# Performance work log

Hardware: AMD Instinct MI355X
Metric: run time of the kernel (lower is better)

The kernel has to match this reference:

```python
import jax, jax.numpy as jnp
import numpy as np

N = 50000        # node_num
E = 1600000      # num edges (avg degree 32)
IN_DIM = 128
OUT_DIM = 64
SLOPE = 0.1      # leaky relu slope_ratio
EPS = 1e-12


def setup_inputs() -> dict:
    key = jax.random.key(0)
    k0, k1, k2, k3 = jax.random.split(key, 4)
    x = jax.random.normal(k0, (N, IN_DIM), dtype=jnp.float32)
    edge_index = jax.random.randint(k1, (2, E), 0, N, dtype=jnp.int64)
    # Linear(in_dim, out_dim) params
    W = jax.random.normal(k2, (OUT_DIM, IN_DIM), dtype=jnp.float32) * (1.0 / np.sqrt(IN_DIM))
    b = jnp.zeros((OUT_DIM,), dtype=jnp.float32)
    # attention vector a: [2*out_dim, 1], kaiming-normal-ish init
    a = jax.random.normal(k3, (2 * OUT_DIM, 1), dtype=jnp.float32) * np.sqrt(2.0 / (2 * OUT_DIM))
    return {"x": x, "edge_index": edge_index, "W": W, "b": b, "a": a}


def reference(x, edge_index, W, b, a):
    # new_embeddings = Linear(x)
    new = x @ W.T + b                          # [N, OUT_DIM]
    src = edge_index[0]
    dst = edge_index[1]
    # cat(new[src], new[dst]) @ a  ==  new[src]@a_src + new[dst]@a_dst (avoids [E, 2*OUT] intermediate)
    a_src = a[:OUT_DIM, 0]                     # [OUT_DIM]
    a_dst = a[OUT_DIM:, 0]                     # [OUT_DIM]
    score = new[src] @ a_src + new[dst] @ a_dst  # [E]
    e = jnp.exp(jax.nn.leaky_relu(score, SLOPE))  # [E]
    # spmm(A, ones) -> per-row sum of edge weights; spmm(A, new) -> weighted aggregation
    row_sum = jax.ops.segment_sum(e, src, num_segments=N)                 # [N]
    results = jax.ops.segment_sum(e[:, None] * new[dst], src, num_segments=N)  # [N, OUT_DIM]
    return results / (row_sum[:, None] + EPS)
```

## Files before the change

### kernel.cpp

```cpp
#include <hip/hip_runtime.h>
#include <hip/hip_bf16.h>

#define NN    50000
#define EE    1600000
#define IND   128
#define OUTD  64
#define SLOPE 0.1f

#define BSH    5
#define BW     32
#define NB     1564
#define NFINE  1568
#define CAP    1408
#define CAPT   6
#define CSH    8
#define NC     196
#define CAP1   8832
#define NBLK1  500
#define CHUNK1 (EE / NBLK1)
#define NSPLIT 4
#define SCAP   (CAP1 / NSPLIT)
#define NLIN   (NN / 16)

typedef __attribute__((ext_vector_type(8))) short short8;
typedef __attribute__((ext_vector_type(4))) float float4v;

union SMem {
    struct {
        ushort xs[16 * 136];
        ushort wt[64 * 136];
        float  newt[16 * 68];
    } lin;
    int h[NC];
};

__global__ __launch_bounds__(256) void fused_lincoarse_kernel(
    const float* __restrict__ x, const float* __restrict__ W,
    const float* __restrict__ bias, const float* __restrict__ a,
    const int* __restrict__ ei, int* __restrict__ gcur1,
    unsigned* __restrict__ ebuf1,
    ushort* __restrict__ nbuf2, float* __restrict__ s_src, float* __restrict__ s_dst)
{
    __shared__ SMem sm;
    const int tid = threadIdx.x;

    if (blockIdx.x < NBLK1) {
        int* h = sm.h;
        for (int i = tid; i < NC; i += 256) h[i] = 0;
        __syncthreads();
        const int base = blockIdx.x * CHUNK1;
        const int4* s4p = (const int4*)(ei + base);
        for (int i = tid; i < CHUNK1 / 4; i += 256) {
            int4 s4 = s4p[i];
            atomicAdd(&h[s4.x >> CSH], 1);
            atomicAdd(&h[s4.y >> CSH], 1);
            atomicAdd(&h[s4.z >> CSH], 1);
            atomicAdd(&h[s4.w >> CSH], 1);
        }
        __syncthreads();
        for (int i = tid; i < NC; i += 256) {
            int c = h[i];
            if (c) h[i] = i * CAP1 + atomicAdd(&gcur1[i * 16], c);
        }
        __syncthreads();
        const int4* d4p = (const int4*)(ei + EE + base);
        for (int i = tid; i < CHUNK1 / 4; i += 256) {
            int4 s4 = s4p[i];
            int4 d4 = d4p[i];
            int p0 = atomicAdd(&h[s4.x >> CSH], 1);
            int p1 = atomicAdd(&h[s4.y >> CSH], 1);
            int p2 = atomicAdd(&h[s4.z >> CSH], 1);
            int p3 = atomicAdd(&h[s4.w >> CSH], 1);
            ebuf1[p0] = ((unsigned)(s4.x & 255) << 16) | (unsigned)d4.x;
            ebuf1[p1] = ((unsigned)(s4.y & 255) << 16) | (unsigned)d4.y;
            ebuf1[p2] = ((unsigned)(s4.z & 255) << 16) | (unsigned)d4.z;
            ebuf1[p3] = ((unsigned)(s4.w & 255) << 16) | (unsigned)d4.w;
        }
        return;
    }

    const int node0 = (blockIdx.x - NBLK1) * 16;
    const float4* W4 = (const float4*)W;
    #pragma unroll
    for (int i = 0; i < 8; ++i) {
        int idx = tid + i * 256;
        float4 wv = W4[idx];
        int n = idx >> 5, k = (idx & 31) * 4;
        ushort4 pk; __hip_bfloat16 h;
        h = __float2bfloat16(wv.x); pk.x = *(ushort*)&h;
        h = __float2bfloat16(wv.y); pk.y = *(ushort*)&h;
        h = __float2bfloat16(wv.z); pk.z = *(ushort*)&h;
        h = __float2bfloat16(wv.w); pk.w = *(ushort*)&h;
        *(ushort4*)&sm.lin.wt[n * 136 + k] = pk;
    }
    const float4* x4 = (const float4*)(x + (size_t)node0 * IND);
    #pragma unroll
    for (int i = 0; i < 2; ++i) {
        int idx = tid + i * 256;
        float4 xv = x4[idx];
        int r = idx >> 5, cc = (idx & 31) * 4;
        ushort4 pk; __hip_bfloat16 h;
        h = __float2bfloat16(xv.x); pk.x = *(ushort*)&h;
        h = __float2bfloat16(xv.y); pk.y = *(ushort*)&h;
        h = __float2bfloat16(xv.z); pk.z = *(ushort*)&h;
        h = __float2bfloat16(xv.w); pk.w = *(ushort*)&h;
        *(ushort4*)&sm.lin.xs[r * 136 + cc] = pk;
    }
    __syncthreads();

    const int w    = tid >> 6;
    const int lane = tid & 63;
    const int q    = lane >> 4;
    const int m16  = lane & 15;
    float4v acc = {0.f, 0.f, 0.f, 0.f};
    #pragma unroll
    for (int kk = 0; kk < IND; kk += 32) {
        short8 af = *(const short8*)&sm.lin.xs[m16 * 136 + kk + q * 8];
        short8 bf = *(const short8*)&sm.lin.wt[(w * 16 + m16) * 136 + kk + q * 8];
        acc = __builtin_amdgcn_mfma_f32_16x16x32_bf16(af, bf, acc, 0, 0, 0);
    }
    const float bv = bias[w * 16 + m16];
    #pragma unroll
    for (int r = 0; r < 4; ++r)
        sm.lin.newt[(q * 4 + r) * 68 + w * 16 + m16] = acc[r] + bv;
    __syncthreads();

    const int nl = tid >> 4;
    const int jg = tid & 15;
    const int j0 = jg * 4;
    float4 va = *(const float4*)&sm.lin.newt[nl * 68 + j0];
    const int n = node0 + nl;
    ushort4 pk;
    { __hip_bfloat16 h;
      h = __float2bfloat16(va.x); pk.x = *(ushort*)&h;
      h = __float2bfloat16(va.y); pk.y = *(ushort*)&h;
      h = __float2bfloat16(va.z); pk.z = *(ushort*)&h;
      h = __float2bfloat16(va.w); pk.w = *(ushort*)&h; }
    *(ushort4*)&nbuf2[(size_t)n * OUTD + j0] = pk;

    float ss = va.x * a[j0]        + va.y * a[j0 + 1]
             + va.z * a[j0 + 2]    + va.w * a[j0 + 3];
    float sd = va.x * a[OUTD + j0]     + va.y * a[OUTD + j0 + 1]
             + va.z * a[OUTD + j0 + 2] + va.w * a[OUTD + j0 + 3];
    #pragma unroll
    for (int m = 1; m < 16; m <<= 1) {
        ss += __shfl_xor(ss, m, 64);
        sd += __shfl_xor(sd, m, 64);
    }
    if (jg == 0) { s_src[n] = ss; s_dst[n] = sd; }
}

__global__ __launch_bounds__(256) void finebin_kernel(
    const unsigned* __restrict__ ebuf1, const int* __restrict__ gcur1,
    int* __restrict__ gcur2, unsigned* __restrict__ ebuf2)
{
    __shared__ unsigned stage[SCAP];
    __shared__ int h[8], lofs[8], grun[8], cur[8];
    const int tid = threadIdx.x;
    const int c   = blockIdx.x >> 2;
    const int sp  = blockIdx.x & 3;
    const int cnt1 = gcur1[c * 16];
    const int seg  = (cnt1 + NSPLIT - 1) / NSPLIT;
    const int lo   = sp * seg;
    const int m    = max(0, min(cnt1, lo + seg) - lo);
    if (tid < 8) h[tid] = 0;
    __syncthreads();
    const unsigned* eb = ebuf1 + (size_t)c * CAP1 + lo;
    for (int i = tid; i < m; i += 256)
        atomicAdd(&h[eb[i] >> 21], 1);
    __syncthreads();
    if (tid == 0) {
        int run = 0;
        #pragma unroll
        for (int f = 0; f < 8; ++f) { lofs[f] = run; run += h[f]; }
    }
    __syncthreads();
    if (tid < 8) {
        cur[tid]  = lofs[tid];
        grun[tid] = atomicAdd(&gcur2[(c * 8 + tid) * 16], h[tid]);
    }
    __syncthreads();
    for (int i = tid; i < m; i += 256) {
        unsigned e = eb[i];
        int pos = atomicAdd(&cur[e >> 21], 1);
        stage[pos] = (((e >> 16) & 31u) << 16) | (e & 0xFFFFu);
    }
    __syncthreads();
    #pragma unroll 1
    for (int f = 0; f < 8; ++f) {
        const int cf = h[f];
        unsigned* dst = ebuf2 + (size_t)(c * 8 + f) * CAP + grun[f];
        const unsigned* sp2 = stage + lofs[f];
        for (int i = tid; i < cf; i += 256) dst[i] = sp2[i];
    }
}

__global__ __launch_bounds__(256) void aggregate_kernel(
    const unsigned* __restrict__ ebuf, const int* __restrict__ gcur,
    const ushort* __restrict__ nbuf2,
    const float* __restrict__ s_src, const float* __restrict__ s_dst,
    float* __restrict__ out)
{
    __shared__ uint2 pairs[CAP];
    __shared__ float ssL[BW];
    __shared__ int cntL[BW], ofs[BW], cur[BW];
    const int tid  = threadIdx.x;
    const int wid  = tid >> 6;
    const int lane = tid & 63;
    const int b    = blockIdx.x;
    const int n0   = b << BSH;
    const uint2* __restrict__ nbufq = (const uint2*)nbuf2;

    if (tid < BW) {
        int n = n0 + tid;
        ssL[tid]  = (n < NN) ? s_src[n] : 0.f;
        cntL[tid] = 0;
    }
    __syncthreads();

    const int cnt = gcur[b * 16];
    const unsigned* eb = ebuf + (size_t)b * CAP;

    unsigned er[CAPT]; float evr[CAPT];
    int nk = 0;
    for (int i = tid; i < cnt; i += 256) {
        unsigned e = eb[i];
        int d  = e & 0xFFFFu;
        int ln = e >> 16;
        float sc = ssL[ln] + s_dst[d];
        float lr = sc > 0.f ? sc : SLOPE * sc;
        er[nk] = e; evr[nk] = __expf(lr); ++nk;
        atomicAdd(&cntL[ln], 1);
    }
    __syncthreads();

    if (wid == 0) {
        int c = (lane < BW) ? cntL[lane] : 0;
        int sc = c;
        #pragma unroll
        for (int m = 1; m < BW; m <<= 1) {
            int v = __shfl_up(sc, m, 64);
            if (lane >= m) sc += v;
        }
        if (lane < BW) { ofs[lane] = sc - c; cur[lane] = sc - c; }
    }
    __syncthreads();

    for (int k = 0; k < nk; ++k) {
        int ln = er[k] >> 16;
        int pos = atomicAdd(&cur[ln], 1);
        pairs[pos] = make_uint2(er[k] & 0xFFFFu, __float_as_uint(evr[k]));
    }
    __syncthreads();

    const int e16 = lane >> 4;
    const int c16 = lane & 15;

    #pragma unroll 1
    for (int t = 0; t < BW / 4; ++t) {
        const int ln  = wid * (BW / 4) + t;
        const int beg = ofs[ln];
        const int len = cntL[ln];

        float a0 = 0.f, a1 = 0.f, a2 = 0.f, a3 = 0.f, es = 0.f;
        int j = 0;
        for (; j + 16 <= len; j += 16) {
            uint2 pA = pairs[beg + j + 0  + e16];
            uint2 pB = pairs[beg + j + 4  + e16];
            uint2 pC = pairs[beg + j + 8  + e16];
            uint2 pD = pairs[beg + j + 12 + e16];
            uint2 gA = nbufq[pA.x * 16 + c16];
            uint2 gB = nbufq[pB.x * 16 + c16];
            uint2 gC = nbufq[pC.x * 16 + c16];
            uint2 gD = nbufq[pD.x * 16 + c16];
            float fA = __uint_as_float(pA.y), fB = __uint_as_float(pB.y);
            float fC = __uint_as_float(pC.y), fD = __uint_as_float(pD.y);
            es += fA + fB + fC + fD;
            a0 = fmaf(fA, __uint_as_float(gA.x << 16), a0);
            a1 = fmaf(fA, __uint_as_float(gA.x & 0xFFFF0000u), a1);
            a2 = fmaf(fA, __uint_as_float(gA.y << 16), a2);
            a3 = fmaf(fA, __uint_as_float(gA.y & 0xFFFF0000u), a3);
            a0 = fmaf(fB, __uint_as_float(gB.x << 16), a0);
            a1 = fmaf(fB, __uint_as_float(gB.x & 0xFFFF0000u), a1);
            a2 = fmaf(fB, __uint_as_float(gB.y << 16), a2);
            a3 = fmaf(fB, __uint_as_float(gB.y & 0xFFFF0000u), a3);
            a0 = fmaf(fC, __uint_as_float(gC.x << 16), a0);
            a1 = fmaf(fC, __uint_as_float(gC.x & 0xFFFF0000u), a1);
            a2 = fmaf(fC, __uint_as_float(gC.y << 16), a2);
            a3 = fmaf(fC, __uint_as_float(gC.y & 0xFFFF0000u), a3);
            a0 = fmaf(fD, __uint_as_float(gD.x << 16), a0);
            a1 = fmaf(fD, __uint_as_float(gD.x & 0xFFFF0000u), a1);
            a2 = fmaf(fD, __uint_as_float(gD.y << 16), a2);
            a3 = fmaf(fD, __uint_as_float(gD.y & 0xFFFF0000u), a3);
        }
        for (; j < len; j += 4) {
            int idx = j + e16;
            uint2 p = pairs[beg + min(idx, len - 1)];
            float f = (idx < len) ? __uint_as_float(p.y) : 0.f;
            uint2 g = nbufq[p.x * 16 + c16];
            es += f;
            a0 = fmaf(f, __uint_as_float(g.x << 16), a0);
            a1 = fmaf(f, __uint_as_float(g.x & 0xFFFF0000u), a1);
            a2 = fmaf(f, __uint_as_float(g.y << 16), a2);
            a3 = fmaf(f, __uint_as_float(g.y & 0xFFFF0000u), a3);
        }
        es += __shfl_xor(es, 16, 64); es += __shfl_xor(es, 32, 64);
        a0 += __shfl_xor(a0, 16, 64); a0 += __shfl_xor(a0, 32, 64);
        a1 += __shfl_xor(a1, 16, 64); a1 += __shfl_xor(a1, 32, 64);
        a2 += __shfl_xor(a2, 16, 64); a2 += __shfl_xor(a2, 32, 64);
        a3 += __shfl_xor(a3, 16, 64); a3 += __shfl_xor(a3, 32, 64);
        const int n = n0 + ln;
        if (e16 == 0 && n < NN) {
            float inv = 1.f / (es + 1e-12f);
            float4 o = make_float4(a0 * inv, a1 * inv, a2 * inv, a3 * inv);
            *(float4*)&out[(size_t)n * OUTD + c16 * 4] = o;
        }
    }
}

extern "C" void kernel_launch(void* const* d_in, const int* in_sizes, int n_in,
                              void* d_out, int out_size, void* d_ws, size_t ws_size,
                              hipStream_t stream) {
    const float* x  = (const float*)d_in[0];
    const int*   ei = (const int*)d_in[1];
    const float* W  = (const float*)d_in[2];
    const float* b  = (const float*)d_in[3];
    const float* a  = (const float*)d_in[4];
    float* out = (float*)d_out;

    ushort*   nbuf2 = (ushort*)d_ws;
    float*    s_src = (float*)(nbuf2 + (size_t)NN * OUTD);
    float*    s_dst = s_src + NN;
    int*      gcur1 = (int*)(s_dst + NN);
    int*      gcur2 = gcur1 + NC * 16;
    unsigned* ebuf1 = (unsigned*)(gcur2 + NFINE * 16);
    unsigned* ebuf2 = ebuf1 + (size_t)NC * CAP1;

    hipMemsetAsync(gcur1, 0, (NC + NFINE) * 16 * sizeof(int), stream);
    fused_lincoarse_kernel<<<NBLK1 + NLIN, 256, 0, stream>>>(
        x, W, b, a, ei, gcur1, ebuf1, nbuf2, s_src, s_dst);
    finebin_kernel<<<NC * NSPLIT, 256, 0, stream>>>(ebuf1, gcur1, gcur2, ebuf2);
    aggregate_kernel<<<NB, 256, 0, stream>>>(ebuf2, gcur2, nbuf2, s_src, s_dst, out);
}
```

Before: 148.5 us.

## Fuse fine binning into aggregation by filtering coarse buckets per sub-block

```diff
diff --git a/kernel.cpp b/kernel.cpp
--- a/kernel.cpp
+++ b/kernel.cpp
@@ -9,18 +9,15 @@
 
 #define BSH    5
 #define BW     32
-#define NB     1564
-#define NFINE  1568
 #define CAP    1408
-#define CAPT   6
 #define CSH    8
 #define NC     196
 #define CAP1   8832
 #define NBLK1  500
 #define CHUNK1 (EE / NBLK1)
-#define NSPLIT 4
-#define SCAP   (CAP1 / NSPLIT)
 #define NLIN   (NN / 16)
+#define CGRID  200
+#define NSUB   8
 
 typedef __attribute__((ext_vector_type(8))) short short8;
 typedef __attribute__((ext_vector_type(4))) float float4v;
@@ -150,53 +147,8 @@
     if (jg == 0) { s_src[n] = ss; s_dst[n] = sd; }
 }
 
-__global__ __launch_bounds__(256) void finebin_kernel(
+__global__ __launch_bounds__(256) void aggregate_kernel(
     const unsigned* __restrict__ ebuf1, const int* __restrict__ gcur1,
-    int* __restrict__ gcur2, unsigned* __restrict__ ebuf2)
-{
-    __shared__ unsigned stage[SCAP];
-    __shared__ int h[8], lofs[8], grun[8], cur[8];
-    const int tid = threadIdx.x;
-    const int c   = blockIdx.x >> 2;
-    const int sp  = blockIdx.x & 3;
-    const int cnt1 = gcur1[c * 16];
-    const int seg  = (cnt1 + NSPLIT - 1) / NSPLIT;
-    const int lo   = sp * seg;
-    const int m    = max(0, min(cnt1, lo + seg) - lo);
-    if (tid < 8) h[tid] = 0;
-    __syncthreads();
-    const unsigned* eb = ebuf1 + (size_t)c * CAP1 + lo;
-    for (int i = tid; i < m; i += 256)
-        atomicAdd(&h[eb[i] >> 21], 1);
-    __syncthreads();
-    if (tid == 0) {
-        int run = 0;
-        #pragma unroll
-        for (int f = 0; f < 8; ++f) { lofs[f] = run; run += h[f]; }
-    }
-    __syncthreads();
-    if (tid < 8) {
-        cur[tid]  = lofs[tid];
-        grun[tid] = atomicAdd(&gcur2[(c * 8 + tid) * 16], h[tid]);
-    }
-    __syncthreads();
-    for (int i = tid; i < m; i += 256) {
-        unsigned e = eb[i];
-        int pos = atomicAdd(&cur[e >> 21], 1);
-        stage[pos] = (((e >> 16) & 31u) << 16) | (e & 0xFFFFu);
-    }
-    __syncthreads();
-    #pragma unroll 1
-    for (int f = 0; f < 8; ++f) {
-        const int cf = h[f];
-        unsigned* dst = ebuf2 + (size_t)(c * 8 + f) * CAP + grun[f];
-        const unsigned* sp2 = stage + lofs[f];
-        for (int i = tid; i < cf; i += 256) dst[i] = sp2[i];
-    }
-}
-
-__global__ __launch_bounds__(256) void aggregate_kernel(
-    const unsigned* __restrict__ ebuf, const int* __restrict__ gcur,
     const ushort* __restrict__ nbuf2,
     const float* __restrict__ s_src, const float* __restrict__ s_dst,
     float* __restrict__ out)
@@ -207,8 +159,10 @@
     const int tid  = threadIdx.x;
     const int wid  = tid >> 6;
     const int lane = tid & 63;
-    const int b    = blockIdx.x;
-    const int n0   = b << BSH;
+    const int c    = blockIdx.x % CGRID;
+    const int sub  = blockIdx.x / CGRID;
+    if (c >= NC) return;
+    const int n0   = (c << CSH) + (sub << BSH);
     const uint2* __restrict__ nbufq = (const uint2*)nbuf2;
 
     if (tid < BW) {
@@ -218,38 +172,39 @@
     }
     __syncthreads();
 
-    const int cnt = gcur[b * 16];
-    const unsigned* eb = ebuf + (size_t)b * CAP;
-
-    unsigned er[CAPT]; float evr[CAPT];
-    int nk = 0;
-    for (int i = tid; i < cnt; i += 256) {
+    const int cnt1 = gcur1[c * 16];
+    const unsigned* eb = ebuf1 + (size_t)c * CAP1;
+    const unsigned subu = (unsigned)sub;
+
+    for (int i = tid; i < cnt1; i += 256) {
         unsigned e = eb[i];
-        int d  = e & 0xFFFFu;
-        int ln = e >> 16;
-        float sc = ssL[ln] + s_dst[d];
-        float lr = sc > 0.f ? sc : SLOPE * sc;
-        er[nk] = e; evr[nk] = __expf(lr); ++nk;
-        atomicAdd(&cntL[ln], 1);
+        if (((e >> 21) & 7u) == subu)
+            atomicAdd(&cntL[(e >> 16) & 31u], 1);
     }
     __syncthreads();
 
     if (wid == 0) {
-        int c = (lane < BW) ? cntL[lane] : 0;
-        int sc = c;
+        int cc = (lane < BW) ? cntL[lane] : 0;
+        int sc = cc;
         #pragma unroll
         for (int m = 1; m < BW; m <<= 1) {
             int v = __shfl_up(sc, m, 64);
             if (lane >= m) sc += v;
         }
-        if (lane < BW) { ofs[lane] = sc - c; cur[lane] = sc - c; }
-    }
-    __syncthreads();
-
-    for (int k = 0; k < nk; ++k) {
-        int ln = er[k] >> 16;
-        int pos = atomicAdd(&cur[ln], 1);
-        pairs[pos] = make_uint2(er[k] & 0xFFFFu, __float_as_uint(evr[k]));
+        if (lane < BW) { ofs[lane] = sc - cc; cur[lane] = sc - cc; }
+    }
+    __syncthreads();
+
+    for (int i = tid; i < cnt1; i += 256) {
+        unsigned e = eb[i];
+        if (((e >> 21) & 7u) == subu) {
+            int ln = (e >> 16) & 31u;
+            int d  = e & 0xFFFFu;
+            float scv = ssL[ln] + s_dst[d];
+            float lr  = scv > 0.f ? scv : SLOPE * scv;
+            int pos = atomicAdd(&cur[ln], 1);
+            pairs[pos] = make_uint2((unsigned)d, __float_as_uint(__expf(lr)));
+        }
     }
     __syncthreads();
 
@@ -332,13 +287,11 @@
     float*    s_src = (float*)(nbuf2 + (size_t)NN * OUTD);
     float*    s_dst = s_src + NN;
     int*      gcur1 = (int*)(s_dst + NN);
-    int*      gcur2 = gcur1 + NC * 16;
-    unsigned* ebuf1 = (unsigned*)(gcur2 + NFINE * 16);
-    unsigned* ebuf2 = ebuf1 + (size_t)NC * CAP1;
-
-    hipMemsetAsync(gcur1, 0, (NC + NFINE) * 16 * sizeof(int), stream);
+    unsigned* ebuf1 = (unsigned*)(gcur1 + NC * 16);
+
+    hipMemsetAsync(gcur1, 0, NC * 16 * sizeof(int), stream);
     fused_lincoarse_kernel<<<NBLK1 + NLIN, 256, 0, stream>>>(
         x, W, b, a, ei, gcur1, ebuf1, nbuf2, s_src, s_dst);
-    finebin_kernel<<<NC * NSPLIT, 256, 0, stream>>>(ebuf1, gcur1, gcur2, ebuf2);
-    aggregate_kernel<<<NB, 256, 0, stream>>>(ebuf2, gcur2, nbuf2, s_src, s_dst, out);
+    aggregate_kernel<<<CGRID * NSUB, 256, 0, stream>>>(
+        ebuf1, gcur1, nbuf2, s_src, s_dst, out);
 }
```

Measured after the change: 157.2 us. +5.9%, slower.
